# Kernel optimization log

Measured on AMD Instinct MI355X. Metric: run time of the kernel, lower is better.

Reference implementation:

```python
import jax, jax.numpy as jnp
import numpy as np

M, N, H, K1, K2, C, B = 100000, 14000, 256, 16, 32, 7, 64
EPS = 1e-8


def setup_inputs() -> dict:
    key = jax.random.key(0)
    ks = jax.random.split(key, 8)
    embeds = jax.random.normal(ks[0], (M, H), dtype=jnp.float32)
    idx = jax.random.randint(ks[1], (N,), 0, M, dtype=jnp.int32)
    neighbors = jax.random.randint(ks[2], (N, K1), 0, M, dtype=jnp.int32)
    neighbors_2hop = jax.random.randint(ks[3], (N, K2), 0, M, dtype=jnp.int32)
    labels = (jnp.arange(N, dtype=jnp.int32) % C)  # perfectly balanced, as averageemb requires
    # prompt params (downstreamprompt weights, xavier-uniform [1,H])
    lim = float(np.sqrt(6.0 / (1 + H)))
    w_self = jax.random.uniform(ks[4], (1, H), jnp.float32, -lim, lim)
    w_n = jax.random.uniform(ks[5], (1, H), jnp.float32, -lim, lim)
    w_n2 = jax.random.uniform(ks[6], (1, H), jnp.float32, -lim, lim)
    # metanet (PromptVector): bottleneck adapter H -> B -> H
    k7, k8 = jax.random.split(ks[7])
    W1 = jax.random.normal(k7, (H, B), jnp.float32) * (1.0 / np.sqrt(H))
    b1 = jnp.zeros((B,), jnp.float32)
    W2 = jax.random.normal(k8, (B, H), jnp.float32) * (1.0 / np.sqrt(B))
    b2 = jnp.zeros((H,), jnp.float32)
    return {"embeds": embeds, "w_self": w_self, "w_n": w_n, "w_n2": w_n2,
            "W1": W1, "b1": b1, "W2": W2, "b2": b2,
            "idx": idx, "neighbors": neighbors, "neighbors_2hop": neighbors_2hop,
            "labels": labels}


def _cos(a, b):
    # torch.cosine_similarity with eps=1e-8 (clamped norms)
    num = jnp.sum(a * b, axis=-1)
    na = jnp.maximum(jnp.sqrt(jnp.sum(a * a, axis=-1)), EPS)
    nb = jnp.maximum(jnp.sqrt(jnp.sum(b * b, axis=-1)), EPS)
    return num / (na * nb)


def reference(embeds, w_self, w_n, w_n2, W1, b1, W2, b2,
              idx, neighbors, neighbors_2hop, labels):
    center = embeds[idx]                         # [N,H]
    ce = w_self * center                         # selfprompt: [N,H]
    nb = jnp.nan_to_num(w_n * embeds[neighbors])              # [N,K1,H]
    nb2 = jnp.nan_to_num(w_n2 * embeds[neighbors_2hop])       # [N,K2,H]
    nb_all = jnp.concatenate([nb, nb2], axis=1)  # [N,K1+K2,H]
    sim = _cos(ce[:, None, :], nb_all)           # [N,K]
    w = jax.nn.softmax(sim, axis=-1)
    weighted_neighbors = jnp.einsum('nk,nkh->nh', w, nb_all)
    inputs = weighted_neighbors + ce             # (dropout = identity at eval)
    prompts = jax.nn.elu(inputs @ W1 + b1) @ W2 + b2  # metanet adapter
    rawret = prompts + ce                        # [N,H]
    # averageemb: per-class mean (labels balanced, N/C per class)
    per_class = N // C
    ave = jax.ops.segment_sum(rawret, labels, num_segments=C) / per_class  # [C,H]
    ret = jax.nn.softmax(_cos(rawret[:, None, :], ave[None, :, :]), axis=1)  # [N,C]
    return ret
```

## Files before the change

### kernel.cpp

```cpp
#include <hip/hip_runtime.h>
#include <math.h>

#define H 256
#define NR 14000
#define K1C 16
#define K2C 32
#define KT 48
#define CC 7
#define EPSF 1e-8f
#define GC1 128
#define CHUNK ((NR + GC1 - 1) / GC1)

__device__ __forceinline__ float rdlane(float v, int l) {
    return __int_as_float(__builtin_amdgcn_readlane(__float_as_int(v), l));
}

__device__ __forceinline__ float dot4(const float4 a, const float4 b) {
    return a.x * b.x + a.y * b.y + a.z * b.z + a.w * b.w;
}

__global__ __launch_bounds__(256) void kA(
    const float* __restrict__ embeds, const float* __restrict__ w_self,
    const float* __restrict__ w_n, const float* __restrict__ w_n2,
    const int* __restrict__ idx, const int* __restrict__ nbr1,
    const int* __restrict__ nbr2, float* __restrict__ inbuf,
    float* __restrict__ cebuf)
{
    const int tid = threadIdx.x;
    const int wv = tid >> 6, lane = tid & 63;
    const int n = blockIdx.x * 4 + wv;
    const int g = lane >> 4, l = lane & 15;
    const int hb = l * 4;

    float4 wn4[4], wn24[4], ce4[4];
    float na2 = 0.f;
    const int cidx = idx[n];
    const float* crow = embeds + (size_t)cidx * H;
#pragma unroll
    for (int j = 0; j < 4; ++j) {
        const float4 wsv = *(const float4*)(w_self + hb + 64 * j);
        wn4[j]  = *(const float4*)(w_n  + hb + 64 * j);
        wn24[j] = *(const float4*)(w_n2 + hb + 64 * j);
        const float4 cv = *(const float4*)(crow + hb + 64 * j);
        float4 ce;
        ce.x = wsv.x * cv.x; ce.y = wsv.y * cv.y;
        ce.z = wsv.z * cv.z; ce.w = wsv.w * cv.w;
        ce4[j] = ce;
        na2 += dot4(ce, ce);
    }
#pragma unroll
    for (int m = 1; m <= 8; m <<= 1) na2 += __shfl_xor(na2, m);
    const float na = fmaxf(sqrtf(na2), EPSF);

    int ridx = 0;
    if (lane < K1C) ridx = nbr1[n * K1C + lane];
    else if (lane < KT) ridx = nbr2[n * K2C + (lane - K1C)];

    float4 acc[4];
#pragma unroll
    for (int j = 0; j < 4; ++j) acc[j] = make_float4(0.f, 0.f, 0.f, 0.f);
    float lsum = 0.f;

#pragma unroll
    for (int kk = 0; kk < 12; ++kk) {
        const int row = __shfl(ridx, kk * 4 + g);
        const float* rp = embeds + (size_t)row * H;
        float num = 0.f, nn = 0.f;
        float4 nb4[4];
#pragma unroll
        for (int j = 0; j < 4; ++j) {
            const float4 ev = *(const float4*)(rp + hb + 64 * j);
            const float4 wv4 = (kk < 4) ? wn4[j] : wn24[j];
            float4 nb;
            nb.x = wv4.x * ev.x; nb.y = wv4.y * ev.y;
            nb.z = wv4.z * ev.z; nb.w = wv4.w * ev.w;
            nb4[j] = nb;
            num += dot4(ce4[j], nb);
            nn  += dot4(nb, nb);
        }
#pragma unroll
        for (int m = 1; m <= 8; m <<= 1) {
            num += __shfl_xor(num, m);
            nn  += __shfl_xor(nn, m);
        }
        const float nbn = fmaxf(sqrtf(nn), EPSF);
        const float sim = num / (nbn * na);
        const float e = __expf(sim - 1.0f);
        lsum += e;
#pragma unroll
        for (int j = 0; j < 4; ++j) {
            acc[j].x += e * nb4[j].x; acc[j].y += e * nb4[j].y;
            acc[j].z += e * nb4[j].z; acc[j].w += e * nb4[j].w;
        }
    }
#pragma unroll
    for (int m = 16; m <= 32; m <<= 1) {
        lsum += __shfl_xor(lsum, m);
#pragma unroll
        for (int j = 0; j < 4; ++j) {
            acc[j].x += __shfl_xor(acc[j].x, m);
            acc[j].y += __shfl_xor(acc[j].y, m);
            acc[j].z += __shfl_xor(acc[j].z, m);
            acc[j].w += __shfl_xor(acc[j].w, m);
        }
    }
    const float rl = 1.0f / lsum;
    if (g == 0) {
        float* ip = inbuf + (size_t)n * H;
        float* cp = cebuf + (size_t)n * H;
#pragma unroll
        for (int j = 0; j < 4; ++j) {
            float4 iv;
            iv.x = acc[j].x * rl + ce4[j].x;
            iv.y = acc[j].y * rl + ce4[j].y;
            iv.z = acc[j].z * rl + ce4[j].z;
            iv.w = acc[j].w * rl + ce4[j].w;
            *(float4*)(ip + hb + 64 * j) = iv;
            *(float4*)(cp + hb + 64 * j) = ce4[j];
        }
    }
}

__global__ __launch_bounds__(256) void kB(
    float* io, const float* __restrict__ cebuf,
    const float* __restrict__ W1, const float* __restrict__ b1,
    const float* __restrict__ W2, const float* __restrict__ b2)
{
    __shared__ float W1T[64 * 256];
    const int tid = threadIdx.x;
    {
        const int b = tid & 63, hblk = tid >> 6;
        for (int hh = 0; hh < 64; ++hh) {
            const int h = hblk * 64 + hh;
            const int chunk = (h >> 2) ^ (b & 15);
            W1T[b * 256 + chunk * 4 + (h & 3)] = W1[h * 64 + b];
        }
    }
    __syncthreads();

    const int wv = tid >> 6, lane = tid & 63;
    const int r0 = (blockIdx.x * 4 + wv) * 8;
    if (r0 >= NR) return;
    const int nr = min(8, NR - r0);

    float4 in4[8];
#pragma unroll
    for (int r = 0; r < 8; ++r) in4[r] = make_float4(0.f, 0.f, 0.f, 0.f);
    for (int r = 0; r < nr; ++r)
        in4[r] = *(const float4*)(io + (size_t)(r0 + r) * H + 4 * lane);

    float hid[8];
    const float bb = b1[lane];
#pragma unroll
    for (int r = 0; r < 8; ++r) hid[r] = bb;

    for (int h4 = 0; h4 < 64; ++h4) {
        const float4 w1v = *(const float4*)(&W1T[lane * 256 + 4 * (h4 ^ (lane & 15))]);
#pragma unroll
        for (int j = 0; j < 4; ++j) {
            const float wj = (j == 0) ? w1v.x : (j == 1) ? w1v.y : (j == 2) ? w1v.z : w1v.w;
#pragma unroll
            for (int r = 0; r < 8; ++r) {
                const float src = (j == 0) ? in4[r].x : (j == 1) ? in4[r].y
                                 : (j == 2) ? in4[r].z : in4[r].w;
                hid[r] += rdlane(src, h4) * wj;
            }
        }
    }
#pragma unroll
    for (int r = 0; r < 8; ++r)
        hid[r] = hid[r] > 0.f ? hid[r] : (__expf(hid[r]) - 1.0f);

    float4 p4[8];
    const float4 b2v = *(const float4*)(b2 + 4 * lane);
#pragma unroll
    for (int r = 0; r < 8; ++r) p4[r] = b2v;
    for (int b = 0; b < 64; ++b) {
        const float4 w2v = *(const float4*)(W2 + b * H + 4 * lane);
#pragma unroll
        for (int r = 0; r < 8; ++r) {
            const float hv = rdlane(hid[r], b);
            p4[r].x += hv * w2v.x; p4[r].y += hv * w2v.y;
            p4[r].z += hv * w2v.z; p4[r].w += hv * w2v.w;
        }
    }
    for (int r = 0; r < nr; ++r) {
        const float4 cev = *(const float4*)(cebuf + (size_t)(r0 + r) * H + 4 * lane);
        float4 ov;
        ov.x = p4[r].x + cev.x; ov.y = p4[r].y + cev.y;
        ov.z = p4[r].z + cev.z; ov.w = p4[r].w + cev.w;
        *(float4*)(io + (size_t)(r0 + r) * H + 4 * lane) = ov;
    }
}

__global__ __launch_bounds__(256) void kC1(
    const float* __restrict__ rawret, const int* __restrict__ labels,
    float* __restrict__ partial)
{
    const int t = threadIdx.x, j = blockIdx.x;
    const int nlo = j * CHUNK;
    const int nhi = min(nlo + CHUNK, NR);
    float acc[CC];
#pragma unroll
    for (int c = 0; c < CC; ++c) acc[c] = 0.f;
    for (int n = nlo; n < nhi; ++n) {
        const int lab = labels[n];
        const float v = rawret[(size_t)n * H + t];
#pragma unroll
        for (int c = 0; c < CC; ++c) acc[c] += (lab == c) ? v : 0.f;
    }
#pragma unroll
    for (int c = 0; c < CC; ++c) partial[(size_t)(j * CC + c) * H + t] = acc[c];
}

__global__ __launch_bounds__(256) void kC2(
    const float* __restrict__ partial, float* __restrict__ ave,
    float* __restrict__ anorm)
{
    const int c = blockIdx.x, t = threadIdx.x;
    float s = 0.f;
    for (int j = 0; j < GC1; ++j) s += partial[(size_t)(j * CC + c) * H + t];
    const float a = s * (1.0f / 2000.0f);
    ave[c * H + t] = a;
    __shared__ float red[256];
    red[t] = a * a;
    __syncthreads();
    for (int m = 128; m > 0; m >>= 1) {
        if (t < m) red[t] += red[t + m];
        __syncthreads();
    }
    if (t == 0) anorm[c] = fmaxf(sqrtf(red[0]), EPSF);
}

__global__ __launch_bounds__(256) void kD(
    const float* __restrict__ rawret, const float* __restrict__ ave,
    const float* __restrict__ anorm, float* __restrict__ out)
{
    const int tid = threadIdx.x;
    const int wv = tid >> 6, lane = tid & 63;
    const int n = blockIdx.x * 4 + wv;
    const float4 r4 = *(const float4*)(rawret + (size_t)n * H + 4 * lane);
    float nr2 = dot4(r4, r4);
#pragma unroll
    for (int m = 1; m <= 32; m <<= 1) nr2 += __shfl_xor(nr2, m);
    const float rn = fmaxf(sqrtf(nr2), EPSF);

    float e[CC];
    float s = 0.f;
#pragma unroll
    for (int c = 0; c < CC; ++c) {
        const float4 a4 = *(const float4*)(ave + c * H + 4 * lane);
        float d = dot4(r4, a4);
#pragma unroll
        for (int m = 1; m <= 32; m <<= 1) d += __shfl_xor(d, m);
        const float sim = d / (rn * anorm[c]);
        e[c] = __expf(sim - 1.0f);
        s += e[c];
    }
    const float rs = 1.0f / s;
    if (lane < CC) {
        float v = e[0];
#pragma unroll
        for (int c = 1; c < CC; ++c) v = (lane == c) ? e[c] : v;
        out[(size_t)n * CC + lane] = v * rs;
    }
}

extern "C" void kernel_launch(void* const* d_in, const int* in_sizes, int n_in,
                              void* d_out, int out_size, void* d_ws, size_t ws_size,
                              hipStream_t stream) {
    const float* embeds = (const float*)d_in[0];
    const float* w_self = (const float*)d_in[1];
    const float* w_n    = (const float*)d_in[2];
    const float* w_n2   = (const float*)d_in[3];
    const float* W1     = (const float*)d_in[4];
    const float* b1     = (const float*)d_in[5];
    const float* W2     = (const float*)d_in[6];
    const float* b2     = (const float*)d_in[7];
    const int* idx      = (const int*)d_in[8];
    const int* nbr1     = (const int*)d_in[9];
    const int* nbr2     = (const int*)d_in[10];
    const int* labels   = (const int*)d_in[11];
    float* out = (float*)d_out;

    float* buf0    = (float*)d_ws;
    float* buf1    = buf0 + (size_t)NR * H;
    float* partial = buf1 + (size_t)NR * H;
    float* ave     = partial + (size_t)GC1 * CC * H;
    float* anorm   = ave + (size_t)CC * H;

    kA<<<NR / 4, 256, 0, stream>>>(embeds, w_self, w_n, w_n2, idx, nbr1, nbr2,
                                   buf0, buf1);
    kB<<<(NR + 31) / 32, 256, 0, stream>>>(buf0, buf1, W1, b1, W2, b2);
    kC1<<<GC1, 256, 0, stream>>>(buf0, labels, partial);
    kC2<<<CC, 256, 0, stream>>>(partial, ave, anorm);
    kD<<<NR / 4, 256, 0, stream>>>(buf0, ave, anorm, out);
}
```

Measured before the change: 381.4 us.

## Gather neighbors from a bf16 copy of embeds and simplify the adapter kernel

Adds a kernel that converts the full 100k×256 embedding table to bf16 in workspace on every call. The neighbor-gather kernel then reads 16 bf16 values per lane instead of fp32, halving the bytes per gathered row. The adapter kernel drops the shared-memory W1 transpose and reads W1 and the inputs straight from global memory, four rows per wave. The conversion pass reads the whole table (about 100 MB) to save gather traffic on only about 670k rows (roughly 680 MB), and bf16 neighbor values lose precision in the similarity and weighted sum.

```diff
diff --git a/kernel.cpp b/kernel.cpp
--- a/kernel.cpp
+++ b/kernel.cpp
@@ -1,8 +1,10 @@
 #include <hip/hip_runtime.h>
+#include <hip/hip_bf16.h>
 #include <math.h>
 
 #define H 256
 #define NR 14000
+#define MR 100000
 #define K1C 16
 #define K2C 32
 #define KT 48
@@ -11,12 +13,122 @@
 #define GC1 128
 #define CHUNK ((NR + GC1 - 1) / GC1)
 
+typedef __attribute__((ext_vector_type(8))) unsigned short ushort8_t;
+
 __device__ __forceinline__ float rdlane(float v, int l) {
     return __int_as_float(__builtin_amdgcn_readlane(__float_as_int(v), l));
 }
 
 __device__ __forceinline__ float dot4(const float4 a, const float4 b) {
     return a.x * b.x + a.y * b.y + a.z * b.z + a.w * b.w;
+}
+
+__device__ __forceinline__ unsigned short f2bf(float x) {
+    __hip_bfloat16 h = __float2bfloat16(x);
+    return *(unsigned short*)&h;
+}
+
+__global__ __launch_bounds__(256) void kE(const float* __restrict__ src,
+                                          unsigned short* __restrict__ dst) {
+    const size_t base = ((size_t)blockIdx.x * 256 + threadIdx.x) * 8;
+    const float4 a = *(const float4*)(src + base);
+    const float4 b = *(const float4*)(src + base + 4);
+    ushort8_t o;
+    o[0] = f2bf(a.x); o[1] = f2bf(a.y); o[2] = f2bf(a.z); o[3] = f2bf(a.w);
+    o[4] = f2bf(b.x); o[5] = f2bf(b.y); o[6] = f2bf(b.z); o[7] = f2bf(b.w);
+    *(ushort8_t*)(dst + base) = o;
+}
+
+__global__ __launch_bounds__(256) void kA2(
+    const float* __restrict__ embeds, const unsigned short* __restrict__ ebf,
+    const float* __restrict__ w_self, const float* __restrict__ w_n,
+    const float* __restrict__ w_n2, const int* __restrict__ idx,
+    const int* __restrict__ nbr1, const int* __restrict__ nbr2,
+    float* __restrict__ inbuf, float* __restrict__ cebuf)
+{
+    const int tid = threadIdx.x;
+    const int wv = tid >> 6, lane = tid & 63;
+    const int n = blockIdx.x * 4 + wv;
+    const int g = lane >> 4, l = lane & 15;
+    const int hb = l * 16;
+
+    float ce[16], wn[16], wn2[16];
+    float na2 = 0.f;
+    const int cidx = idx[n];
+    const float* crow = embeds + (size_t)cidx * H + hb;
+#pragma unroll
+    for (int j = 0; j < 4; ++j) {
+        const float4 wsv  = *(const float4*)(w_self + hb + 4 * j);
+        const float4 wnv  = *(const float4*)(w_n    + hb + 4 * j);
+        const float4 wn2v = *(const float4*)(w_n2   + hb + 4 * j);
+        const float4 cv   = *(const float4*)(crow + 4 * j);
+        wn[4*j+0] = wnv.x;  wn[4*j+1] = wnv.y;  wn[4*j+2] = wnv.z;  wn[4*j+3] = wnv.w;
+        wn2[4*j+0] = wn2v.x; wn2[4*j+1] = wn2v.y; wn2[4*j+2] = wn2v.z; wn2[4*j+3] = wn2v.w;
+        ce[4*j+0] = wsv.x * cv.x; ce[4*j+1] = wsv.y * cv.y;
+        ce[4*j+2] = wsv.z * cv.z; ce[4*j+3] = wsv.w * cv.w;
+        na2 += ce[4*j+0]*ce[4*j+0] + ce[4*j+1]*ce[4*j+1]
+             + ce[4*j+2]*ce[4*j+2] + ce[4*j+3]*ce[4*j+3];
+    }
+#pragma unroll
+    for (int m = 1; m <= 8; m <<= 1) na2 += __shfl_xor(na2, m);
+    const float na = fmaxf(sqrtf(na2), EPSF);
+
+    int ridx = 0;
+    if (lane < K1C) ridx = nbr1[n * K1C + lane];
+    else if (lane < KT) ridx = nbr2[n * K2C + (lane - K1C)];
+
+    float acc[16];
+#pragma unroll
+    for (int i = 0; i < 16; ++i) acc[i] = 0.f;
+    float lsum = 0.f;
+
+#pragma unroll
+    for (int kk = 0; kk < 12; ++kk) {
+        const int row = __shfl(ridx, kk * 4 + g);
+        const unsigned short* rp = ebf + (size_t)row * H + hb;
+        const ushort8_t e0 = *(const ushort8_t*)(rp);
+        const ushort8_t e1 = *(const ushort8_t*)(rp + 8);
+        float nb[16];
+#pragma unroll
+        for (int i = 0; i < 8; ++i) {
+            nb[i]     = __uint_as_float((unsigned)e0[i] << 16);
+            nb[8 + i] = __uint_as_float((unsigned)e1[i] << 16);
+        }
+        float num = 0.f, nn = 0.f;
+#pragma unroll
+        for (int i = 0; i < 16; ++i) {
+            const float w = (kk < 4) ? wn[i] : wn2[i];
+            nb[i] *= w;
+            num += ce[i] * nb[i];
+            nn  += nb[i] * nb[i];
+        }
+#pragma unroll
+        for (int m = 1; m <= 8; m <<= 1) {
+            num += __shfl_xor(num, m);
+            nn  += __shfl_xor(nn, m);
+        }
+        const float nbn = fmaxf(sqrtf(nn), EPSF);
+        const float e = __expf(num / (nbn * na) - 1.0f);
+        lsum += e;
+#pragma unroll
+        for (int i = 0; i < 16; ++i) acc[i] += e * nb[i];
+    }
+#pragma unroll
+    for (int m = 16; m <= 32; m <<= 1) {
+        lsum += __shfl_xor(lsum, m);
+#pragma unroll
+        for (int i = 0; i < 16; ++i) acc[i] += __shfl_xor(acc[i], m);
+    }
+    const float rl = 1.0f / lsum;
+    if (g == 0) {
+        float* ip = inbuf + (size_t)n * H + hb;
+        float* cp = cebuf + (size_t)n * H + hb;
+#pragma unroll
+        for (int i = 0; i < 16; ++i) {
+            ip[i] = acc[i] * rl + ce[i];
+            cp[i] = ce[i];
+        }
+    }
 }
 
 __global__ __launch_bounds__(256) void kA(
@@ -84,8 +196,7 @@
             nn  += __shfl_xor(nn, m);
         }
         const float nbn = fmaxf(sqrtf(nn), EPSF);
-        const float sim = num / (nbn * na);
-        const float e = __expf(sim - 1.0f);
+        const float e = __expf(num / (nbn * na) - 1.0f);
         lsum += e;
 #pragma unroll
         for (int j = 0; j < 4; ++j) {
@@ -121,70 +232,49 @@
     }
 }
 
-__global__ __launch_bounds__(256) void kB(
-    float* io, const float* __restrict__ cebuf,
+__global__ __launch_bounds__(256) void kB2(
+    float* __restrict__ io, const float* __restrict__ cebuf,
     const float* __restrict__ W1, const float* __restrict__ b1,
     const float* __restrict__ W2, const float* __restrict__ b2)
 {
-    __shared__ float W1T[64 * 256];
     const int tid = threadIdx.x;
-    {
-        const int b = tid & 63, hblk = tid >> 6;
-        for (int hh = 0; hh < 64; ++hh) {
-            const int h = hblk * 64 + hh;
-            const int chunk = (h >> 2) ^ (b & 15);
-            W1T[b * 256 + chunk * 4 + (h & 3)] = W1[h * 64 + b];
-        }
-    }
-    __syncthreads();
-
     const int wv = tid >> 6, lane = tid & 63;
-    const int r0 = (blockIdx.x * 4 + wv) * 8;
-    if (r0 >= NR) return;
-    const int nr = min(8, NR - r0);
-
-    float4 in4[8];
-#pragma unroll
-    for (int r = 0; r < 8; ++r) in4[r] = make_float4(0.f, 0.f, 0.f, 0.f);
-    for (int r = 0; r < nr; ++r)
-        in4[r] = *(const float4*)(io + (size_t)(r0 + r) * H + 4 * lane);
-
-    float hid[8];
+    const int r0 = __builtin_amdgcn_readfirstlane((blockIdx.x * 4 + wv) * 4);
+    const float* inb = io + (size_t)r0 * H;
+
+    float hid[4];
     const float bb = b1[lane];
 #pragma unroll
-    for (int r = 0; r < 8; ++r) hid[r] = bb;
-
-    for (int h4 = 0; h4 < 64; ++h4) {
-        const float4 w1v = *(const float4*)(&W1T[lane * 256 + 4 * (h4 ^ (lane & 15))]);
-#pragma unroll
-        for (int j = 0; j < 4; ++j) {
-            const float wj = (j == 0) ? w1v.x : (j == 1) ? w1v.y : (j == 2) ? w1v.z : w1v.w;
-#pragma unroll
-            for (int r = 0; r < 8; ++r) {
-                const float src = (j == 0) ? in4[r].x : (j == 1) ? in4[r].y
-                                 : (j == 2) ? in4[r].z : in4[r].w;
-                hid[r] += rdlane(src, h4) * wj;
-            }
-        }
-    }
-#pragma unroll
-    for (int r = 0; r < 8; ++r)
+    for (int r = 0; r < 4; ++r) hid[r] = bb;
+
+#pragma unroll 8
+    for (int h = 0; h < 256; ++h) {
+        const float w1v = W1[h * 64 + lane];
+        hid[0] += inb[h]           * w1v;
+        hid[1] += inb[H + h]       * w1v;
+        hid[2] += inb[2 * H + h]   * w1v;
+        hid[3] += inb[3 * H + h]   * w1v;
+    }
+#pragma unroll
+    for (int r = 0; r < 4; ++r)
         hid[r] = hid[r] > 0.f ? hid[r] : (__expf(hid[r]) - 1.0f);
 
-    float4 p4[8];
+    float4 p4[4];
     const float4 b2v = *(const float4*)(b2 + 4 * lane);
 #pragma unroll
-    for (int r = 0; r < 8; ++r) p4[r] = b2v;
+    for (int r = 0; r < 4; ++r) p4[r] = b2v;
+#pragma unroll 4
     for (int b = 0; b < 64; ++b) {
         const float4 w2v = *(const float4*)(W2 + b * H + 4 * lane);
 #pragma unroll
-        for (int r = 0; r < 8; ++r) {
+        for (int r = 0; r < 4; ++r) {
             const float hv = rdlane(hid[r], b);
             p4[r].x += hv * w2v.x; p4[r].y += hv * w2v.y;
             p4[r].z += hv * w2v.z; p4[r].w += hv * w2v.w;
         }
     }
-    for (int r = 0; r < nr; ++r) {
+#pragma unroll
+    for (int r = 0; r < 4; ++r) {
         const float4 cev = *(const float4*)(cebuf + (size_t)(r0 + r) * H + 4 * lane);
         float4 ov;
         ov.x = p4[r].x + cev.x; ov.y = p4[r].y + cev.y;
@@ -219,6 +309,7 @@
 {
     const int c = blockIdx.x, t = threadIdx.x;
     float s = 0.f;
+#pragma unroll 8
     for (int j = 0; j < GC1; ++j) s += partial[(size_t)(j * CC + c) * H + t];
     const float a = s * (1.0f / 2000.0f);
     ave[c * H + t] = a;
@@ -288,10 +379,19 @@
     float* partial = buf1 + (size_t)NR * H;
     float* ave     = partial + (size_t)GC1 * CC * H;
     float* anorm   = ave + (size_t)CC * H;
-
-    kA<<<NR / 4, 256, 0, stream>>>(embeds, w_self, w_n, w_n2, idx, nbr1, nbr2,
-                                   buf0, buf1);
-    kB<<<(NR + 31) / 32, 256, 0, stream>>>(buf0, buf1, W1, b1, W2, b2);
+    unsigned short* ebf = (unsigned short*)(anorm + 8);
+
+    const size_t need = ((char*)ebf - (char*)d_ws) + (size_t)MR * H * 2;
+
+    if (ws_size >= need) {
+        kE<<<(MR * H) / (256 * 8), 256, 0, stream>>>(embeds, ebf);
+        kA2<<<NR / 4, 256, 0, stream>>>(embeds, ebf, w_self, w_n, w_n2,
+                                        idx, nbr1, nbr2, buf0, buf1);
+    } else {
+        kA<<<NR / 4, 256, 0, stream>>>(embeds, w_self, w_n, w_n2,
+                                       idx, nbr1, nbr2, buf0, buf1);
+    }
+    kB2<<<NR / 16, 256, 0, stream>>>(buf0, buf1, W1, b1, W2, b2);
     kC1<<<GC1, 256, 0, stream>>>(buf0, labels, partial);
     kC2<<<CC, 256, 0, stream>>>(partial, ave, anorm);
     kD<<<NR / 4, 256, 0, stream>>>(buf0, ave, anorm, out);
```

After: 328.4 us. 13.9% less time.
